# Kernel optimization log

Hardware: AMD Instinct MI355X
Metric: run time of the kernel (lower is better)

Reference implementation:

```python
import jax, jax.numpy as jnp
import numpy as np

B, S, D, H = 2, 2048, 1024, 16
DH = D // H


def setup_inputs() -> dict:
    key = jax.random.key(0)
    ks = jax.random.split(key, 6)
    scale = 1.0 / np.sqrt(D)
    x = jax.random.normal(ks[0], (B, S, D), dtype=jnp.float32)
    mask = jnp.tril(jnp.ones((S, S), dtype=jnp.int32))  # causal 0/1 mask
    Wq = jax.random.normal(ks[1], (D, D), dtype=jnp.float32) * scale
    Wk = jax.random.normal(ks[2], (D, D), dtype=jnp.float32) * scale
    Wv = jax.random.normal(ks[3], (D, D), dtype=jnp.float32) * scale
    Wo = jax.random.normal(ks[4], (D, D), dtype=jnp.float32) * scale
    z = jnp.zeros((D,), dtype=jnp.float32)
    return {"x": x, "mask": mask, "Wq": Wq, "bq": z, "Wk": Wk, "bk": z,
            "Wv": Wv, "bv": z, "Wo": Wo, "bo": z}


def reference(x, mask, Wq, bq, Wk, bk, Wv, bv, Wo, bo):
    # Linear projections (torch Linear: x @ W.T + b; here W stored as [in, out])
    Q = x @ Wq + bq
    K = x @ Wk + bk
    V = x @ Wv + bv
    # [B, S, D] -> [B, H, S, DH]
    Q = Q.reshape(B, S, H, DH).transpose(0, 2, 1, 3)
    K = K.reshape(B, S, H, DH).transpose(0, 2, 1, 3)
    V = V.reshape(B, S, H, DH).transpose(0, 2, 1, 3)
    # scores: [B, H, S, S]
    attn = jnp.einsum('bhqd,bhkd->bhqk', Q, K) / jnp.sqrt(jnp.float32(DH))
    attn = jnp.where(mask == 0, jnp.float32(-1e9), attn)
    scores = jax.nn.softmax(attn, axis=-1)
    # dropout is identity in eval mode
    out = jnp.einsum('bhqk,bhkd->bhqd', scores, V)
    out = out.transpose(0, 2, 1, 3).reshape(B, S, D)
    return out @ Wo + bo
```

## Files before the change

### kernel.cpp

```cpp
#include <hip/hip_runtime.h>
#include <hip/hip_bf16.h>


typedef short bf16x8 __attribute__((ext_vector_type(8)));
typedef float f32x4  __attribute__((ext_vector_type(4)));
typedef short s16x4  __attribute__((ext_vector_type(4)));

#define BB 2
#define SS 2048
#define DD 1024
#define HH 16
#define DHH 64

__device__ __forceinline__ unsigned short f2bf(float f) {
    unsigned u = __builtin_bit_cast(unsigned, f);
    u += 0x7FFFu + ((u >> 16) & 1u);
    return (unsigned short)(u >> 16);
}
__device__ __forceinline__ unsigned short f2bf_trunc(float f) {
    return (unsigned short)(__builtin_bit_cast(unsigned, f) >> 16);
}
__device__ __forceinline__ void cp16(const unsigned short* g, unsigned short* l) {
    __builtin_amdgcn_global_load_lds(
        (const __attribute__((address_space(1))) unsigned int*)(g),
        (__attribute__((address_space(3))) unsigned int*)(l), 16, 0, 0);
}

__global__ __launch_bounds__(256) void prep(
    const float* __restrict__ x,
    const float* __restrict__ w0, const float* __restrict__ w1,
    const float* __restrict__ w2, const float* __restrict__ w3,
    unsigned short* __restrict__ xbf, unsigned short* __restrict__ wt) {
    __shared__ float tile[64][65];
    const int bid = blockIdx.x;
    const int tid = threadIdx.x;
    if (bid < 4096) {
        int i = (bid * 256 + tid) * 4;
        float4 v = *reinterpret_cast<const float4*>(x + i);
        s16x4 p;
        p[0] = (short)f2bf(v.x); p[1] = (short)f2bf(v.y);
        p[2] = (short)f2bf(v.z); p[3] = (short)f2bf(v.w);
        *reinterpret_cast<s16x4*>(xbf + i) = p;
        return;
    }
    const int tb = bid - 4096;
    const int z  = tb >> 8;
    const int bx = (tb & 15) * 64, by = ((tb >> 4) & 15) * 64;
    const float* src = z == 0 ? w0 : z == 1 ? w1 : z == 2 ? w2 : w3;
    unsigned short* out = wt + (size_t)z * (DD * DD);
    const int tx = tid & 63, ty = tid >> 6;
    #pragma unroll
    for (int i = 0; i < 64; i += 4)
        tile[ty + i][tx] = src[(size_t)(by + ty + i) * DD + bx + tx];
    __syncthreads();
    #pragma unroll
    for (int i = 0; i < 64; i += 4)
        out[(size_t)(bx + ty + i) * DD + by + tx] = f2bf(tile[tx][ty + i]);
}

__global__ __launch_bounds__(512, 2) void gemm_qkv(
    const unsigned short* __restrict__ A, const unsigned short* __restrict__ Wt,
    const float* __restrict__ b0, const float* __restrict__ b1,
    const float* __restrict__ b2,
    unsigned short* __restrict__ d0, unsigned short* __restrict__ d1,
    unsigned short* __restrict__ d2) {
    __shared__ __align__(16) unsigned short As_[2][256 * 64];
    __shared__ __align__(16) unsigned short Bs_[2][192 * 64];

    const int tid  = threadIdx.x;
    const int lane = tid & 63;
    const int w    = tid >> 6;
    const int col  = lane & 15;
    const int quad = lane >> 4;
    const int wr   = w >> 2;
    const int wc   = w & 3;

    const int flat = blockIdx.y * 16 + blockIdx.x;
    const int swz  = (flat & 7) * 32 + (flat >> 3);
    const int mb   = (swz >> 4) * 256;
    const int nb   = (swz & 15) * 192;

    const int r8 = lane >> 3, gg = lane & 7;
    const int srcoff = ((gg ^ r8) * 8);
    const int cswz = col & 7;
    const int pos0 = (quad       ^ cswz) * 8;
    const int pos1 = ((4 + quad) ^ cswz) * 8;

    f32x4 acc[8][3];
    #pragma unroll
    for (int i = 0; i < 8; i++)
        #pragma unroll
        for (int j = 0; j < 3; j++) acc[i][j] = (f32x4){0.f, 0.f, 0.f, 0.f};

    auto stage = [&](int b, int kt) {
        #pragma unroll
        for (int i = 0; i < 4; i++) {
            int rb = w * 32 + i * 8;
            cp16(A + (size_t)(mb + rb + r8) * 1024 + kt + srcoff,
                 As_[b] + rb * 64);
        }
        #pragma unroll
        for (int i = 0; i < 3; i++) {
            int rb = w * 24 + i * 8;
            cp16(Wt + (size_t)(nb + rb + r8) * 1024 + kt + srcoff,
                 Bs_[b] + rb * 64);
        }
    };

    int cur = 0;
    stage(0, 0);
    __syncthreads();

    for (int kt = 0; kt < 1024; kt += 64) {
        if (kt + 64 < 1024) stage(cur ^ 1, kt + 64);
        const unsigned short* Ab = As_[cur];
        const unsigned short* Bb = Bs_[cur];
        bf16x8 bq0[3], bq1[3];
        #pragma unroll
        for (int j = 0; j < 3; j++) {
            const unsigned short* bp = Bb + (wc * 48 + j * 16 + col) * 64;
            bq0[j] = *reinterpret_cast<const bf16x8*>(bp + pos0);
            bq1[j] = *reinterpret_cast<const bf16x8*>(bp + pos1);
        }
        #pragma unroll
        for (int mi = 0; mi < 8; mi++) {
            const unsigned short* ap = Ab + (wr * 128 + mi * 16 + col) * 64;
            bf16x8 a0 = *reinterpret_cast<const bf16x8*>(ap + pos0);
            bf16x8 a1 = *reinterpret_cast<const bf16x8*>(ap + pos1);
            #pragma unroll
            for (int j = 0; j < 3; j++) {
                acc[mi][j] = __builtin_amdgcn_mfma_f32_16x16x32_bf16(a0, bq0[j], acc[mi][j], 0, 0, 0);
                acc[mi][j] = __builtin_amdgcn_mfma_f32_16x16x32_bf16(a1, bq1[j], acc[mi][j], 0, 0, 0);
            }
        }
        __syncthreads();
        cur ^= 1;
    }

    const float QSCALE = 0.125f * 1.44269504f;
    #pragma unroll
    for (int mi = 0; mi < 8; mi++) {
        int mg = mb + wr * 128 + mi * 16 + quad * 4;
        #pragma unroll
        for (int nj = 0; nj < 3; nj++) {
            int ng = nb + wc * 48 + nj * 16 + col;
            int sel = ng >> 10, n2 = ng & 1023;
            int h = n2 >> 6, dd2 = n2 & 63;
            int b = mg >> 11, s = mg & 2047;
            int bh = b * HH + h;
            const float* bp = sel == 0 ? b0 : sel == 1 ? b1 : b2;
            float bbv = bp[n2];
            if (sel == 0) {
                #pragma unroll
                for (int r = 0; r < 4; r++)
                    d0[((size_t)bh * SS + s + r) * DHH + dd2] = f2bf((acc[mi][nj][r] + bbv) * QSCALE);
            } else if (sel == 1) {
                #pragma unroll
                for (int r = 0; r < 4; r++)
                    d1[((size_t)bh * SS + s + r) * DHH + dd2] = f2bf(acc[mi][nj][r] + bbv);
            } else {
                s16x4 pack;
                #pragma unroll
                for (int r = 0; r < 4; r++) pack[r] = (short)f2bf(acc[mi][nj][r] + bbv);
                *reinterpret_cast<s16x4*>(d2 + ((size_t)bh * DHH + dd2) * SS + s) = pack;
            }
        }
    }
}

__global__ __launch_bounds__(256) void gemm_out(
    const unsigned short* __restrict__ A, const unsigned short* __restrict__ Wt,
    const float* __restrict__ b0, float* __restrict__ d0f) {
    __shared__ __align__(16) unsigned short As_[2][128 * 64];
    __shared__ __align__(16) unsigned short Bs_[2][128 * 64];

    const int tid  = threadIdx.x;
    const int lane = tid & 63;
    const int w    = tid >> 6;
    const int col  = lane & 15;
    const int quad = lane >> 4;
    const int wm   = (w >> 1) * 64;
    const int wn   = (w & 1) * 64;

    const int flat = blockIdx.y * 8 + blockIdx.x;
    const int swz  = (flat & 7) * 32 + (flat >> 3);
    const int mb   = (swz >> 3) * 128;
    const int nb   = (swz & 7) * 128;

    const int r8 = lane >> 3, gg = lane & 7;
    const int srcoff = ((gg ^ r8) * 8);
    const int cswz = col & 7;
    const int pos0 = (quad       ^ cswz) * 8;
    const int pos1 = ((4 + quad) ^ cswz) * 8;

    f32x4 acc[4][4];
    #pragma unroll
    for (int i = 0; i < 4; i++)
        #pragma unroll
        for (int j = 0; j < 4; j++) acc[i][j] = (f32x4){0.f, 0.f, 0.f, 0.f};

    auto stage = [&](int b, int kt) {
        #pragma unroll
        for (int it = 0; it < 4; it++) {
            int row = w * 32 + it * 8;
            cp16(A  + (size_t)(mb + row + r8) * 1024 + kt + srcoff, As_[b] + row * 64);
            cp16(Wt + (size_t)(nb + row + r8) * 1024 + kt + srcoff, Bs_[b] + row * 64);
        }
    };

    int cur = 0;
    stage(0, 0);
    __syncthreads();

    for (int kt = 0; kt < 1024; kt += 64) {
        if (kt + 64 < 1024) stage(cur ^ 1, kt + 64);
        const unsigned short* Ab = As_[cur];
        const unsigned short* Bb = Bs_[cur];
        bf16x8 bq0[4], bq1[4];
        #pragma unroll
        for (int j = 0; j < 4; j++) {
            const unsigned short* bp = Bb + (wn + j * 16 + col) * 64;
            bq0[j] = *reinterpret_cast<const bf16x8*>(bp + pos0);
            bq1[j] = *reinterpret_cast<const bf16x8*>(bp + pos1);
        }
        #pragma unroll
        for (int i = 0; i < 4; i++) {
            const unsigned short* ap = Ab + (wm + i * 16 + col) * 64;
            bf16x8 a0 = *reinterpret_cast<const bf16x8*>(ap + pos0);
            bf16x8 a1 = *reinterpret_cast<const bf16x8*>(ap + pos1);
            #pragma unroll
            for (int j = 0; j < 4; j++) {
                acc[i][j] = __builtin_amdgcn_mfma_f32_16x16x32_bf16(a0, bq0[j], acc[i][j], 0, 0, 0);
                acc[i][j] = __builtin_amdgcn_mfma_f32_16x16x32_bf16(a1, bq1[j], acc[i][j], 0, 0, 0);
            }
        }
        __syncthreads();
        cur ^= 1;
    }

    #pragma unroll
    for (int i = 0; i < 4; i++) {
        int mg = mb + wm + i * 16 + quad * 4;
        #pragma unroll
        for (int j = 0; j < 4; j++) {
            int ng = nb + wn + j * 16 + col;
            float bbv = b0[ng];
            #pragma unroll
            for (int r = 0; r < 4; r++)
                d0f[(size_t)(mg + r) * 1024 + ng] = acc[i][j][r] + bbv;
        }
    }
}

__global__ __launch_bounds__(256, 4) void attn(
    const unsigned short* __restrict__ Q, const unsigned short* __restrict__ K,
    const unsigned short* __restrict__ Vt, unsigned short* __restrict__ O) {
    __shared__ __align__(16) unsigned short Ks[2][64 * 64];
    __shared__ __align__(16) unsigned short Vs[2][64 * 64];

    const int tid  = threadIdx.x;
    const int lane = tid & 63;
    const int w    = tid >> 6;
    const int col  = lane & 15;
    const int quad = lane >> 4;
    const int bh   = blockIdx.x & 31;
    const int qt   = 31 - (blockIdx.x >> 5);
    const int qb   = qt * 64;
    const int r8 = lane >> 3, gg = lane & 7;
    const int srcoff = ((gg ^ r8) * 8);
    const int cswz = col & 7;
    const int pos0 = (quad       ^ cswz) * 8;
    const int pos1 = ((4 + quad) ^ cswz) * 8;

    bf16x8 onesf;
    #pragma unroll
    for (int j = 0; j < 8; j++) onesf[j] = (col == 0) ? (short)0x3F80 : (short)0;

    const int qrow = qb + w * 16 + col;
    const size_t qbase = ((size_t)bh * SS + qrow) * DHH;
    bf16x8 qlo = *reinterpret_cast<const bf16x8*>(Q + qbase + quad * 8);
    bf16x8 qhi = *reinterpret_cast<const bf16x8*>(Q + qbase + 32 + quad * 8);

    f32x4 o[5];
    #pragma unroll
    for (int d = 0; d < 5; d++) o[d] = (f32x4){0.f, 0.f, 0.f, 0.f};
    float m_i = -1e30f;

    const int ntiles = qt + 1;
    for (int t0 = 0; t0 < ntiles; t0 += 2) {
        const bool two = (t0 + 1 < ntiles);
        __syncthreads();
        #pragma unroll
        for (int it = 0; it < 2; it++) {
            int drow = w * 16 + it * 8;
            int skey = (w >> 1) * 32 + it * 16 + (r8 >> 2) * 8 + (w & 1) * 4 + (r8 & 3);
            cp16(K  + ((size_t)bh * SS + t0 * 64 + skey) * DHH + srcoff,
                 Ks[0] + drow * 64);
            cp16(Vt + ((size_t)bh * DHH + drow + r8) * SS + t0 * 64 + srcoff,
                 Vs[0] + drow * 64);
        }
        if (two) {
            #pragma unroll
            for (int it = 0; it < 2; it++) {
                int drow = w * 16 + it * 8;
                int skey = (w >> 1) * 32 + it * 16 + (r8 >> 2) * 8 + (w & 1) * 4 + (r8 & 3);
                cp16(K  + ((size_t)bh * SS + (t0 + 1) * 64 + skey) * DHH + srcoff,
                     Ks[1] + drow * 64);
                cp16(Vt + ((size_t)bh * DHH + drow + r8) * SS + (t0 + 1) * 64 + srcoff,
                     Vs[1] + drow * 64);
            }
        }
        __syncthreads();

        f32x4 sc[8];
        #pragma unroll
        for (int nt = 0; nt < 4; nt++) {
            int krow = nt * 16 + col;
            bf16x8 klo = *reinterpret_cast<const bf16x8*>(Ks[0] + krow * 64 + pos0);
            bf16x8 khi = *reinterpret_cast<const bf16x8*>(Ks[0] + krow * 64 + pos1);
            f32x4 z = (f32x4){0.f, 0.f, 0.f, 0.f};
            z = __builtin_amdgcn_mfma_f32_16x16x32_bf16(klo, qlo, z, 0, 0, 0);
            z = __builtin_amdgcn_mfma_f32_16x16x32_bf16(khi, qhi, z, 0, 0, 0);
            sc[nt] = z;
        }
        if (two) {
            #pragma unroll
            for (int nt = 0; nt < 4; nt++) {
                int krow = nt * 16 + col;
                bf16x8 klo = *reinterpret_cast<const bf16x8*>(Ks[1] + krow * 64 + pos0);
                bf16x8 khi = *reinterpret_cast<const bf16x8*>(Ks[1] + krow * 64 + pos1);
                f32x4 z = (f32x4){0.f, 0.f, 0.f, 0.f};
                z = __builtin_amdgcn_mfma_f32_16x16x32_bf16(klo, qlo, z, 0, 0, 0);
                z = __builtin_amdgcn_mfma_f32_16x16x32_bf16(khi, qhi, z, 0, 0, 0);
                sc[4 + nt] = z;
            }
        }
        if (t0 == qt || (two && t0 + 1 == qt)) {
            const int sb = (t0 == qt) ? 0 : 4;
            const int tb = (t0 == qt) ? t0 : t0 + 1;
            #pragma unroll
            for (int nt = 0; nt < 4; nt++) {
                #pragma unroll
                for (int r = 0; r < 4; r++) {
                    int kg = tb * 64 + (nt >> 1) * 32 + quad * 8 + (nt & 1) * 4 + r;
                    if (kg > qrow) sc[sb + nt][r] = -3.0e38f;
                }
            }
        }
        float mx = fmaxf(fmaxf(sc[0][0], sc[0][1]), fmaxf(sc[0][2], sc[0][3]));
        #pragma unroll
        for (int nt = 1; nt < 4; nt++)
            mx = fmaxf(mx, fmaxf(fmaxf(sc[nt][0], sc[nt][1]), fmaxf(sc[nt][2], sc[nt][3])));
        if (two) {
            #pragma unroll
            for (int nt = 4; nt < 8; nt++)
                mx = fmaxf(mx, fmaxf(fmaxf(sc[nt][0], sc[nt][1]), fmaxf(sc[nt][2], sc[nt][3])));
        }
        mx = fmaxf(mx, __shfl_xor(mx, 16));
        mx = fmaxf(mx, __shfl_xor(mx, 32));
        float mnew = fmaxf(m_i, mx);
        bool upd = (mnew > m_i);
        if (__any(upd)) {
            float delta = m_i - mnew;
            #pragma unroll
            for (int r = 0; r < 4; r++) {
                float a = exp2f(__shfl(delta, quad * 4 + r));
                #pragma unroll
                for (int d = 0; d < 5; d++) o[d][r] *= a;
            }
        }
        m_i = mnew;

        {
            bf16x8 pf0, pf1;
            #pragma unroll
            for (int j = 0; j < 8; j++) {
                pf0[j] = (short)f2bf_trunc(exp2f(sc[(j >> 2)][j & 3] - mnew));
                pf1[j] = (short)f2bf_trunc(exp2f(sc[2 + (j >> 2)][j & 3] - mnew));
            }
            #pragma unroll
            for (int dt = 0; dt < 4; dt++) {
                int rv = dt * 16 + col;
                bf16x8 vf0 = *reinterpret_cast<const bf16x8*>(Vs[0] + rv * 64 + pos0);
                bf16x8 vf1 = *reinterpret_cast<const bf16x8*>(Vs[0] + rv * 64 + pos1);
                o[dt] = __builtin_amdgcn_mfma_f32_16x16x32_bf16(pf0, vf0, o[dt], 0, 0, 0);
                o[dt] = __builtin_amdgcn_mfma_f32_16x16x32_bf16(pf1, vf1, o[dt], 0, 0, 0);
            }
            o[4] = __builtin_amdgcn_mfma_f32_16x16x32_bf16(pf0, onesf, o[4], 0, 0, 0);
            o[4] = __builtin_amdgcn_mfma_f32_16x16x32_bf16(pf1, onesf, o[4], 0, 0, 0);
        }
        if (two) {
            bf16x8 pf0, pf1;
            #pragma unroll
            for (int j = 0; j < 8; j++) {
                pf0[j] = (short)f2bf_trunc(exp2f(sc[4 + (j >> 2)][j & 3] - mnew));
                pf1[j] = (short)f2bf_trunc(exp2f(sc[6 + (j >> 2)][j & 3] - mnew));
            }
            #pragma unroll
            for (int dt = 0; dt < 4; dt++) {
                int rv = dt * 16 + col;
                bf16x8 vf0 = *reinterpret_cast<const bf16x8*>(Vs[1] + rv * 64 + pos0);
                bf16x8 vf1 = *reinterpret_cast<const bf16x8*>(Vs[1] + rv * 64 + pos1);
                o[dt] = __builtin_amdgcn_mfma_f32_16x16x32_bf16(pf0, vf0, o[dt], 0, 0, 0);
                o[dt] = __builtin_amdgcn_mfma_f32_16x16x32_bf16(pf1, vf1, o[dt], 0, 0, 0);
            }
            o[4] = __builtin_amdgcn_mfma_f32_16x16x32_bf16(pf0, onesf, o[4], 0, 0, 0);
            o[4] = __builtin_amdgcn_mfma_f32_16x16x32_bf16(pf1, onesf, o[4], 0, 0, 0);
        }
    }

    #pragma unroll
    for (int r = 0; r < 4; r++) {
        float lv = __shfl(o[4][r], lane & 48);
        float inv = 1.0f / lv;
        int sq = qb + w * 16 + quad * 4 + r;
        size_t base = ((size_t)(bh >> 4) * SS + sq) * DD + (size_t)(bh & 15) * DHH;
        #pragma unroll
        for (int dt = 0; dt < 4; dt++)
            O[base + dt * 16 + col] = f2bf(o[dt][r] * inv);
    }
}

extern "C" void kernel_launch(void* const* d_in, const int* in_sizes, int n_in,
                              void* d_out, int out_size, void* d_ws, size_t ws_size,
                              hipStream_t stream) {
    (void)in_sizes; (void)n_in; (void)out_size; (void)ws_size;
    const float* x  = (const float*)d_in[0];
    const float* Wq = (const float*)d_in[2];
    const float* bq = (const float*)d_in[3];
    const float* Wk = (const float*)d_in[4];
    const float* bk = (const float*)d_in[5];
    const float* Wv = (const float*)d_in[6];
    const float* bv = (const float*)d_in[7];
    const float* Wo = (const float*)d_in[8];
    const float* bo = (const float*)d_in[9];
    float* out = (float*)d_out;

    char* ws = (char*)d_ws;
    unsigned short* xbf = (unsigned short*)(ws);
    unsigned short* qws = (unsigned short*)(ws + ((size_t)8  << 20));
    unsigned short* kws = (unsigned short*)(ws + ((size_t)16 << 20));
    unsigned short* vws = (unsigned short*)(ws + ((size_t)24 << 20));
    unsigned short* wt  = (unsigned short*)(ws + ((size_t)32 << 20));
    unsigned short* ows = xbf;

    prep<<<dim3(5120), 256, 0, stream>>>(x, Wq, Wk, Wv, Wo, xbf, wt);
    gemm_qkv<<<dim3(16, 16), 512, 0, stream>>>(xbf, wt, bq, bk, bv,
                                               qws, kws, vws);
    attn<<<dim3(1024), 256, 0, stream>>>(qws, kws, vws, ows);
    gemm_out<<<dim3(8, 32), 256, 0, stream>>>(ows, wt + (size_t)3 * 1024 * 1024,
                                              bo, out);
}
```

Measured before the change: 190.2 us.

## Prefetch next K/V tiles during softmax and interleave QKV GEMM LDS reads

The attention kernel now stages the next pair of K/V tiles into shared memory right after the QK^T MFMAs, so global loads overlap the softmax and PV work. V gets a quad buffer so the prefetch does not clobber the tile still being read. Separately, the QKV projection GEMM splits each k-step into four phases with barriers and s_setprio around MFMA clusters, to interleave LDS reads with matrix ops across waves. The change adds 16KB of LDS per attention block, which may cut occupancy, and more barriers per iteration.

```diff
diff --git a/kernel.cpp b/kernel.cpp
--- a/kernel.cpp
+++ b/kernel.cpp
@@ -115,23 +115,34 @@
         if (kt + 64 < 1024) stage(cur ^ 1, kt + 64);
         const unsigned short* Ab = As_[cur];
         const unsigned short* Bb = Bs_[cur];
-        bf16x8 bq0[3], bq1[3];
-        #pragma unroll
-        for (int j = 0; j < 3; j++) {
-            const unsigned short* bp = Bb + (wc * 48 + j * 16 + col) * 64;
-            bq0[j] = *reinterpret_cast<const bf16x8*>(bp + pos0);
-            bq1[j] = *reinterpret_cast<const bf16x8*>(bp + pos1);
-        }
-        #pragma unroll
-        for (int mi = 0; mi < 8; mi++) {
-            const unsigned short* ap = Ab + (wr * 128 + mi * 16 + col) * 64;
-            bf16x8 a0 = *reinterpret_cast<const bf16x8*>(ap + pos0);
-            bf16x8 a1 = *reinterpret_cast<const bf16x8*>(ap + pos1);
+        #pragma unroll
+        for (int p = 0; p < 4; p++) {
+            bf16x8 af0[2], af1[2], bq0[3], bq1[3];
+            #pragma unroll
+            for (int i = 0; i < 2; i++) {
+                const unsigned short* ap = Ab + (wr * 128 + p * 32 + i * 16 + col) * 64;
+                af0[i] = *reinterpret_cast<const bf16x8*>(ap + pos0);
+                af1[i] = *reinterpret_cast<const bf16x8*>(ap + pos1);
+            }
             #pragma unroll
             for (int j = 0; j < 3; j++) {
-                acc[mi][j] = __builtin_amdgcn_mfma_f32_16x16x32_bf16(a0, bq0[j], acc[mi][j], 0, 0, 0);
-                acc[mi][j] = __builtin_amdgcn_mfma_f32_16x16x32_bf16(a1, bq1[j], acc[mi][j], 0, 0, 0);
-            }
+                const unsigned short* bp = Bb + (wc * 48 + j * 16 + col) * 64;
+                bq0[j] = *reinterpret_cast<const bf16x8*>(bp + pos0);
+                bq1[j] = *reinterpret_cast<const bf16x8*>(bp + pos1);
+            }
+            __builtin_amdgcn_s_barrier();
+            __builtin_amdgcn_s_setprio(1);
+            #pragma unroll
+            for (int i = 0; i < 2; i++)
+                #pragma unroll
+                for (int j = 0; j < 3; j++) {
+                    acc[p * 2 + i][j] = __builtin_amdgcn_mfma_f32_16x16x32_bf16(
+                        af0[i], bq0[j], acc[p * 2 + i][j], 0, 0, 0);
+                    acc[p * 2 + i][j] = __builtin_amdgcn_mfma_f32_16x16x32_bf16(
+                        af1[i], bq1[j], acc[p * 2 + i][j], 0, 0, 0);
+                }
+            __builtin_amdgcn_s_setprio(0);
+            if (p < 3) __builtin_amdgcn_s_barrier();
         }
         __syncthreads();
         cur ^= 1;
@@ -256,7 +267,7 @@
     const unsigned short* __restrict__ Q, const unsigned short* __restrict__ K,
     const unsigned short* __restrict__ Vt, unsigned short* __restrict__ O) {
     __shared__ __align__(16) unsigned short Ks[2][64 * 64];
-    __shared__ __align__(16) unsigned short Vs[2][64 * 64];
+    __shared__ __align__(16) unsigned short Vs[4][64 * 64];
 
     const int tid  = threadIdx.x;
     const int lane = tid & 63;
@@ -286,31 +297,32 @@
     for (int d = 0; d < 5; d++) o[d] = (f32x4){0.f, 0.f, 0.f, 0.f};
     float m_i = -1e30f;
 
-    const int ntiles = qt + 1;
-    for (int t0 = 0; t0 < ntiles; t0 += 2) {
-        const bool two = (t0 + 1 < ntiles);
-        __syncthreads();
+    auto stageK = [&](int slot, int t) {
         #pragma unroll
         for (int it = 0; it < 2; it++) {
             int drow = w * 16 + it * 8;
             int skey = (w >> 1) * 32 + it * 16 + (r8 >> 2) * 8 + (w & 1) * 4 + (r8 & 3);
-            cp16(K  + ((size_t)bh * SS + t0 * 64 + skey) * DHH + srcoff,
-                 Ks[0] + drow * 64);
-            cp16(Vt + ((size_t)bh * DHH + drow + r8) * SS + t0 * 64 + srcoff,
-                 Vs[0] + drow * 64);
-        }
-        if (two) {
-            #pragma unroll
-            for (int it = 0; it < 2; it++) {
-                int drow = w * 16 + it * 8;
-                int skey = (w >> 1) * 32 + it * 16 + (r8 >> 2) * 8 + (w & 1) * 4 + (r8 & 3);
-                cp16(K  + ((size_t)bh * SS + (t0 + 1) * 64 + skey) * DHH + srcoff,
-                     Ks[1] + drow * 64);
-                cp16(Vt + ((size_t)bh * DHH + drow + r8) * SS + (t0 + 1) * 64 + srcoff,
-                     Vs[1] + drow * 64);
-            }
-        }
-        __syncthreads();
+            cp16(K + ((size_t)bh * SS + t * 64 + skey) * DHH + srcoff,
+                 Ks[slot] + drow * 64);
+        }
+    };
+    auto stageV = [&](int slot, int t) {
+        #pragma unroll
+        for (int it = 0; it < 2; it++) {
+            int drow = w * 16 + it * 8;
+            cp16(Vt + ((size_t)bh * DHH + drow + r8) * SS + t * 64 + srcoff,
+                 Vs[slot] + drow * 64);
+        }
+    };
+
+    const int ntiles = qt + 1;
+    stageK(0, 0); stageV(0, 0);
+    if (1 < ntiles) { stageK(1, 1); stageV(1, 1); }
+    __syncthreads();
+
+    for (int t0 = 0; t0 < ntiles; t0 += 2) {
+        const bool two = (t0 + 1 < ntiles);
+        const int vb = (t0 >> 1) & 1;
 
         f32x4 sc[8];
         #pragma unroll
@@ -335,6 +347,13 @@
                 sc[4 + nt] = z;
             }
         }
+        __syncthreads();
+
+        if (t0 + 2 < ntiles) {
+            stageK(0, t0 + 2); stageV((vb ^ 1) * 2, t0 + 2);
+            if (t0 + 3 < ntiles) { stageK(1, t0 + 3); stageV((vb ^ 1) * 2 + 1, t0 + 3); }
+        }
+
         if (t0 == qt || (two && t0 + 1 == qt)) {
             const int sb = (t0 == qt) ? 0 : 4;
             const int tb = (t0 == qt) ? t0 : t0 + 1;
@@ -378,11 +397,12 @@
                 pf0[j] = (short)f2bf_trunc(exp2f(sc[(j >> 2)][j & 3] - mnew));
                 pf1[j] = (short)f2bf_trunc(exp2f(sc[2 + (j >> 2)][j & 3] - mnew));
             }
+            const unsigned short* V0 = Vs[vb * 2];
             #pragma unroll
             for (int dt = 0; dt < 4; dt++) {
                 int rv = dt * 16 + col;
-                bf16x8 vf0 = *reinterpret_cast<const bf16x8*>(Vs[0] + rv * 64 + pos0);
-                bf16x8 vf1 = *reinterpret_cast<const bf16x8*>(Vs[0] + rv * 64 + pos1);
+                bf16x8 vf0 = *reinterpret_cast<const bf16x8*>(V0 + rv * 64 + pos0);
+                bf16x8 vf1 = *reinterpret_cast<const bf16x8*>(V0 + rv * 64 + pos1);
                 o[dt] = __builtin_amdgcn_mfma_f32_16x16x32_bf16(pf0, vf0, o[dt], 0, 0, 0);
                 o[dt] = __builtin_amdgcn_mfma_f32_16x16x32_bf16(pf1, vf1, o[dt], 0, 0, 0);
             }
@@ -396,17 +416,19 @@
                 pf0[j] = (short)f2bf_trunc(exp2f(sc[4 + (j >> 2)][j & 3] - mnew));
                 pf1[j] = (short)f2bf_trunc(exp2f(sc[6 + (j >> 2)][j & 3] - mnew));
             }
+            const unsigned short* V1 = Vs[vb * 2 + 1];
             #pragma unroll
             for (int dt = 0; dt < 4; dt++) {
                 int rv = dt * 16 + col;
-                bf16x8 vf0 = *reinterpret_cast<const bf16x8*>(Vs[1] + rv * 64 + pos0);
-                bf16x8 vf1 = *reinterpret_cast<const bf16x8*>(Vs[1] + rv * 64 + pos1);
+                bf16x8 vf0 = *reinterpret_cast<const bf16x8*>(V1 + rv * 64 + pos0);
+                bf16x8 vf1 = *reinterpret_cast<const bf16x8*>(V1 + rv * 64 + pos1);
                 o[dt] = __builtin_amdgcn_mfma_f32_16x16x32_bf16(pf0, vf0, o[dt], 0, 0, 0);
                 o[dt] = __builtin_amdgcn_mfma_f32_16x16x32_bf16(pf1, vf1, o[dt], 0, 0, 0);
             }
             o[4] = __builtin_amdgcn_mfma_f32_16x16x32_bf16(pf0, onesf, o[4], 0, 0, 0);
             o[4] = __builtin_amdgcn_mfma_f32_16x16x32_bf16(pf1, onesf, o[4], 0, 0, 0);
         }
+        __syncthreads();
     }
 
     #pragma unroll
```

New measurement: 205.8 us. +8.2%, slower.

## Phase QKV GEMM k-loop with barriers and setprio, add setprio to attention MFMAs

Applied to the files above, without the earlier changes.

The QKV GEMM inner loop is split into four phases. Each phase loads its A and B fragments, then all waves hit a barrier and run their MFMA bursts at raised wave priority, so the waves in a workgroup move in lockstep between LDS-read and MFMA phases. The attention kernel wraps its QK and PV MFMA sections in s_setprio so matrix work is favoured over other waves. The GEMM block index swizzle is dropped in favour of a plain row-major block mapping, which may hurt L2 reuse, and the extra barriers add sync cost. B fragments are now reloaded from LDS four times per k-step.

```diff
diff --git a/kernel.cpp b/kernel.cpp
--- a/kernel.cpp
+++ b/kernel.cpp
@@ -74,11 +74,8 @@
     const int quad = lane >> 4;
     const int wr   = w >> 2;
     const int wc   = w & 3;
-
-    const int flat = blockIdx.y * 16 + blockIdx.x;
-    const int swz  = (flat & 7) * 32 + (flat >> 3);
-    const int mb   = (swz >> 4) * 256;
-    const int nb   = (swz & 15) * 192;
+    const int mb   = blockIdx.y * 256;
+    const int nb   = blockIdx.x * 192;
 
     const int r8 = lane >> 3, gg = lane & 7;
     const int srcoff = ((gg ^ r8) * 8);
@@ -115,23 +112,34 @@
         if (kt + 64 < 1024) stage(cur ^ 1, kt + 64);
         const unsigned short* Ab = As_[cur];
         const unsigned short* Bb = Bs_[cur];
-        bf16x8 bq0[3], bq1[3];
-        #pragma unroll
-        for (int j = 0; j < 3; j++) {
-            const unsigned short* bp = Bb + (wc * 48 + j * 16 + col) * 64;
-            bq0[j] = *reinterpret_cast<const bf16x8*>(bp + pos0);
-            bq1[j] = *reinterpret_cast<const bf16x8*>(bp + pos1);
-        }
-        #pragma unroll
-        for (int mi = 0; mi < 8; mi++) {
-            const unsigned short* ap = Ab + (wr * 128 + mi * 16 + col) * 64;
-            bf16x8 a0 = *reinterpret_cast<const bf16x8*>(ap + pos0);
-            bf16x8 a1 = *reinterpret_cast<const bf16x8*>(ap + pos1);
+        #pragma unroll
+        for (int p = 0; p < 4; p++) {
+            bf16x8 af0[2], af1[2], bq0[3], bq1[3];
+            #pragma unroll
+            for (int i = 0; i < 2; i++) {
+                const unsigned short* ap = Ab + (wr * 128 + p * 32 + i * 16 + col) * 64;
+                af0[i] = *reinterpret_cast<const bf16x8*>(ap + pos0);
+                af1[i] = *reinterpret_cast<const bf16x8*>(ap + pos1);
+            }
             #pragma unroll
             for (int j = 0; j < 3; j++) {
-                acc[mi][j] = __builtin_amdgcn_mfma_f32_16x16x32_bf16(a0, bq0[j], acc[mi][j], 0, 0, 0);
-                acc[mi][j] = __builtin_amdgcn_mfma_f32_16x16x32_bf16(a1, bq1[j], acc[mi][j], 0, 0, 0);
-            }
+                const unsigned short* bp = Bb + (wc * 48 + j * 16 + col) * 64;
+                bq0[j] = *reinterpret_cast<const bf16x8*>(bp + pos0);
+                bq1[j] = *reinterpret_cast<const bf16x8*>(bp + pos1);
+            }
+            __builtin_amdgcn_s_barrier();
+            __builtin_amdgcn_s_setprio(1);
+            #pragma unroll
+            for (int i = 0; i < 2; i++)
+                #pragma unroll
+                for (int j = 0; j < 3; j++) {
+                    acc[p * 2 + i][j] = __builtin_amdgcn_mfma_f32_16x16x32_bf16(
+                        af0[i], bq0[j], acc[p * 2 + i][j], 0, 0, 0);
+                    acc[p * 2 + i][j] = __builtin_amdgcn_mfma_f32_16x16x32_bf16(
+                        af1[i], bq1[j], acc[p * 2 + i][j], 0, 0, 0);
+                }
+            __builtin_amdgcn_s_setprio(0);
+            if (p < 3) __builtin_amdgcn_s_barrier();
         }
         __syncthreads();
         cur ^= 1;
@@ -313,6 +321,7 @@
         __syncthreads();
 
         f32x4 sc[8];
+        __builtin_amdgcn_s_setprio(1);
         #pragma unroll
         for (int nt = 0; nt < 4; nt++) {
             int krow = nt * 16 + col;
@@ -335,6 +344,7 @@
                 sc[4 + nt] = z;
             }
         }
+        __builtin_amdgcn_s_setprio(0);
         if (t0 == qt || (two && t0 + 1 == qt)) {
             const int sb = (t0 == qt) ? 0 : 4;
             const int tb = (t0 == qt) ? t0 : t0 + 1;
@@ -378,6 +388,7 @@
                 pf0[j] = (short)f2bf_trunc(exp2f(sc[(j >> 2)][j & 3] - mnew));
                 pf1[j] = (short)f2bf_trunc(exp2f(sc[2 + (j >> 2)][j & 3] - mnew));
             }
+            __builtin_amdgcn_s_setprio(1);
             #pragma unroll
             for (int dt = 0; dt < 4; dt++) {
                 int rv = dt * 16 + col;
@@ -388,6 +399,7 @@
             }
             o[4] = __builtin_amdgcn_mfma_f32_16x16x32_bf16(pf0, onesf, o[4], 0, 0, 0);
             o[4] = __builtin_amdgcn_mfma_f32_16x16x32_bf16(pf1, onesf, o[4], 0, 0, 0);
+            __builtin_amdgcn_s_setprio(0);
         }
         if (two) {
             bf16x8 pf0, pf1;
@@ -396,6 +408,7 @@
                 pf0[j] = (short)f2bf_trunc(exp2f(sc[4 + (j >> 2)][j & 3] - mnew));
                 pf1[j] = (short)f2bf_trunc(exp2f(sc[6 + (j >> 2)][j & 3] - mnew));
             }
+            __builtin_amdgcn_s_setprio(1);
             #pragma unroll
             for (int dt = 0; dt < 4; dt++) {
                 int rv = dt * 16 + col;
@@ -406,6 +419,7 @@
             }
             o[4] = __builtin_amdgcn_mfma_f32_16x16x32_bf16(pf0, onesf, o[4], 0, 0, 0);
             o[4] = __builtin_amdgcn_mfma_f32_16x16x32_bf16(pf1, onesf, o[4], 0, 0, 0);
+            __builtin_amdgcn_s_setprio(0);
         }
     }
 
```

Result: slower. 201.8 us (+6.1%).
